# Kernel tuning notes

Measured on AMD Instinct MI355X. Metric: run time of the kernel, lower is better.

## Reference

```python
import jax, jax.numpy as jnp
import numpy as np

TEMPERATURE = 0.07
NEG_INF_FILL = -1e9  # matches torch fill_diagonal_(-1000000000.0)


def setup_inputs() -> dict:
    key = jax.random.key(0)
    feats = jax.random.normal(key, (6144, 768), dtype=jnp.float32)
    return {"feats": feats}


def reference(feats):
    # L2-normalize rows (torch F.normalize uses eps=1e-12 clamp on the norm)
    norm = jnp.maximum(jnp.linalg.norm(feats, axis=1, keepdims=True), 1e-12)
    f = feats / norm
    N = f.shape[0]
    sim = jnp.matmul(f, f.T) / TEMPERATURE            # [N, N]
    eye = jnp.eye(N, dtype=bool)
    sim = jnp.where(eye, NEG_INF_FILL, sim)           # fill diagonal
    labels = jnp.arange(N) // 3                       # 3 views per slice
    pos = (labels[:, None] == labels[None, :]) & ~eye  # positives, self excluded
    # masked logsumexp over positives via weights b (grad-safe masking)
    numerator = jax.scipy.special.logsumexp(sim, axis=1, b=pos.astype(sim.dtype))
    denominator = jax.scipy.special.logsumexp(sim, axis=1)
    loss = jnp.sum(-(numerator - denominator)) / N
    return loss
```

## Files before the change

kernel.cpp:

```cpp
#include <hip/hip_runtime.h>

#define NN 6144
#define DD 768
#define NB 48
#define NTILES 1176
#define INV_T 14.285714285714286f
#define CMAX  14.285714285714286f

typedef int i32x4 __attribute__((ext_vector_type(4)));
typedef int i32x8 __attribute__((ext_vector_type(8)));
typedef float f32x4_t __attribute__((ext_vector_type(4)));

__device__ __forceinline__ void load_lds16(const void* g, void* l) {
    __builtin_amdgcn_global_load_lds((__attribute__((address_space(1))) void*)g,
                                     (__attribute__((address_space(3))) void*)l,
                                     16, 0, 0);
}

__global__ void norm_kernel(const float* __restrict__ feats,
                            unsigned int* __restrict__ fb8,
                            float* __restrict__ den_num) {
    const int wid = threadIdx.x >> 6;
    const int lane = threadIdx.x & 63;
    const int row = blockIdx.x * 4 + wid;

    if (threadIdx.x < 8) den_num[blockIdx.x * 8 + threadIdx.x] = 0.0f;

    const float4* src = (const float4*)(feats + (size_t)row * DD);
    float4 v[3];
    float ss = 0.0f;
#pragma unroll
    for (int i = 0; i < 3; ++i) {
        v[i] = src[lane + i * 64];
        ss += v[i].x * v[i].x + v[i].y * v[i].y + v[i].z * v[i].z + v[i].w * v[i].w;
    }
#pragma unroll
    for (int m = 32; m >= 1; m >>= 1) ss += __shfl_xor(ss, m);
    const float sc = 1.0f / fmaxf(sqrtf(ss), 1e-12f);

#pragma unroll
    for (int i = 0; i < 3; ++i) {
        unsigned int w = 0;
        w = __builtin_amdgcn_cvt_pk_fp8_f32(v[i].x * sc, v[i].y * sc, w, 0);
        w = __builtin_amdgcn_cvt_pk_fp8_f32(v[i].z * sc, v[i].w * sc, w, 1);
        fb8[(size_t)row * 192 + lane + i * 64] = w;
    }
}

__global__ __launch_bounds__(256, 2) void gemm_expsum_kernel(
        const unsigned char* __restrict__ fb8,
        float* __restrict__ den_sum, float* __restrict__ num_sum) {
    __shared__ __align__(16) char sA0[128 * 128];
    __shared__ __align__(16) char sA1[128 * 128];
    __shared__ __align__(16) char sB0[128 * 128];
    __shared__ __align__(16) char sB1[128 * 128];

    int rem = blockIdx.x;
    int bi = 0, rowlen = NB;
    while (rem >= rowlen) { rem -= rowlen; rowlen--; bi++; }
    const int bj = bi + rem;
    const bool isdiag = (bi == bj);
    const bool neardiag = (bj - bi) <= 1;
    const int i0 = bi * 128;
    const int j0 = bj * 128;

    const int t = threadIdx.x;
    const int lane = t & 63;
    const int wid = t >> 6;
    const int wm = wid >> 1;
    const int wn = wid & 1;

    const int srow = t >> 3;
    const int scb = ((t & 7) ^ (srow & 7)) * 16;
    const unsigned char* gA = fb8 + (size_t)(i0 + srow) * DD + scb;
    const unsigned char* gB = fb8 + (size_t)(j0 + srow) * DD + scb;
    const int ldsoff = wid * 1024;

    f32x4_t acc[4][4];
    const f32x4_t zz = {0.0f, 0.0f, 0.0f, 0.0f};
#pragma unroll
    for (int mi = 0; mi < 4; ++mi)
#pragma unroll
        for (int ni = 0; ni < 4; ++ni) acc[mi][ni] = zz;

    const int q = lane >> 4;
    const int mrow = lane & 15;
    const int x7 = lane & 7;
    const int c0 = ((q << 1) ^ x7) << 4;
    const int c1 = (((q << 1) | 1) ^ x7) << 4;

#define STAGE(dstA, dstB, k0)                                                 \
    {                                                                         \
        _Pragma("unroll")                                                     \
        for (int i = 0; i < 4; ++i) {                                         \
            load_lds16(gA + (size_t)(i * 32) * DD + (k0), (dstA) + ldsoff + i * 4096); \
            load_lds16(gB + (size_t)(i * 32) * DD + (k0), (dstB) + ldsoff + i * 4096); \
        }                                                                     \
    }

#define COMPUTE(srcA, srcB)                                                   \
    {                                                                         \
        i32x8 af[4];                                                          \
        _Pragma("unroll")                                                     \
        for (int mi = 0; mi < 4; ++mi) {                                      \
            const char* p = (srcA) + (wm * 64 + mi * 16 + mrow) * 128;        \
            i32x4 lo = *(const i32x4*)(p + c0);                               \
            i32x4 hi = *(const i32x4*)(p + c1);                               \
            af[mi] = __builtin_shufflevector(lo, hi, 0, 1, 2, 3, 4, 5, 6, 7); \
        }                                                                     \
        _Pragma("unroll")                                                     \
        for (int ni = 0; ni < 4; ++ni) {                                      \
            const char* p = (srcB) + (wn * 64 + ni * 16 + mrow) * 128;        \
            i32x4 lo = *(const i32x4*)(p + c0);                               \
            i32x4 hi = *(const i32x4*)(p + c1);                               \
            i32x8 bf = __builtin_shufflevector(lo, hi, 0, 1, 2, 3, 4, 5, 6, 7); \
            _Pragma("unroll")                                                 \
            for (int mi = 0; mi < 4; ++mi)                                    \
                acc[mi][ni] = __builtin_amdgcn_mfma_scale_f32_16x16x128_f8f6f4( \
                    af[mi], bf, acc[mi][ni], 0, 0,                            \
                    0, 0x7F7F7F7F, 0, 0x7F7F7F7F);                            \
        }                                                                     \
    }

    STAGE(sA0, sB0, 0);
    __syncthreads();

#pragma unroll 1
    for (int kb = 0; kb < 2; ++kb) {
        const int k0 = kb * 256;
        STAGE(sA1, sB1, k0 + 128);
        COMPUTE(sA0, sB0);
        __syncthreads();
        STAGE(sA0, sB0, k0 + 256);
        COMPUTE(sA1, sB1);
        __syncthreads();
    }
    STAGE(sA1, sB1, 640);
    COMPUTE(sA0, sB0);
    __syncthreads();
    COMPUTE(sA1, sB1);

#undef STAGE
#undef COMPUTE

    const int colb = j0 + wn * 64 + mrow;
    const int rowb = i0 + wm * 64 + (q << 2);
    float cs[4] = {0.f, 0.f, 0.f, 0.f};
    float csn[4] = {0.f, 0.f, 0.f, 0.f};
#pragma unroll
    for (int mi = 0; mi < 4; ++mi) {
        float rsv[4] = {0.f, 0.f, 0.f, 0.f};
        float rsn[4] = {0.f, 0.f, 0.f, 0.f};
#pragma unroll
        for (int ni = 0; ni < 4; ++ni) {
            const int col = colb + ni * 16;
#pragma unroll
            for (int r = 0; r < 4; ++r) {
                const int row = rowb + mi * 16 + r;
                float e = __expf(__builtin_fmaf(acc[mi][ni][r], INV_T, -CMAX));
                if (isdiag && row == col) e = 0.0f;
                rsv[r] += e;
                cs[ni] += e;
                if (neardiag && (row / 3 == col / 3) && row != col) {
                    rsn[r] += e;
                    csn[ni] += e;
                }
            }
        }
#pragma unroll
        for (int r = 0; r < 4; ++r) {
            float v = rsv[r];
            v += __shfl_xor(v, 8);
            v += __shfl_xor(v, 4);
            v += __shfl_xor(v, 2);
            v += __shfl_xor(v, 1);
            if (mrow == 0) atomicAdd(&den_sum[rowb + mi * 16 + r], v);
        }
        if (neardiag) {
#pragma unroll
            for (int r = 0; r < 4; ++r) {
                float v = rsn[r];
                v += __shfl_xor(v, 8);
                v += __shfl_xor(v, 4);
                v += __shfl_xor(v, 2);
                v += __shfl_xor(v, 1);
                if (mrow == 0) atomicAdd(&num_sum[rowb + mi * 16 + r], v);
            }
        }
    }
    if (!isdiag) {
#pragma unroll
        for (int ni = 0; ni < 4; ++ni) {
            float v = cs[ni];
            v += __shfl_xor(v, 16);
            v += __shfl_xor(v, 32);
            if (q == 0) atomicAdd(&den_sum[colb + ni * 16], v);
        }
        if (neardiag) {
#pragma unroll
            for (int ni = 0; ni < 4; ++ni) {
                float v = csn[ni];
                v += __shfl_xor(v, 16);
                v += __shfl_xor(v, 32);
                if (q == 0) atomicAdd(&num_sum[colb + ni * 16], v);
            }
        }
    }
}

__global__ void finalize_kernel(const float* __restrict__ den_sum,
                                const float* __restrict__ num_sum,
                                float* __restrict__ out) {
    float local = 0.0f;
    for (int i = threadIdx.x; i < NN; i += 256) {
        local += logf(den_sum[i]) - logf(num_sum[i]);
    }
#pragma unroll
    for (int m = 32; m >= 1; m >>= 1) local += __shfl_xor(local, m);
    __shared__ float ws[4];
    if ((threadIdx.x & 63) == 0) ws[threadIdx.x >> 6] = local;
    __syncthreads();
    if (threadIdx.x == 0) out[0] = (ws[0] + ws[1] + ws[2] + ws[3]) / (float)NN;
}

extern "C" void kernel_launch(void* const* d_in, const int* in_sizes, int n_in,
                              void* d_out, int out_size, void* d_ws, size_t ws_size,
                              hipStream_t stream) {
    const float* feats = (const float*)d_in[0];
    float* out = (float*)d_out;

    char* ws = (char*)d_ws;
    unsigned int* fb8 = (unsigned int*)ws;
    float* den_num    = (float*)(ws + 4718592);
    float* den_sum    = den_num;
    float* num_sum    = den_num + NN;

    norm_kernel<<<NN / 4, 256, 0, stream>>>(feats, fb8, den_num);
    gemm_expsum_kernel<<<NTILES, 256, 0, stream>>>((const unsigned char*)fb8,
                                                   den_sum, num_sum);
    finalize_kernel<<<1, 256, 0, stream>>>(den_sum, num_sum, out);
}
```

Before: 115.6 us.

## Swizzle tile order into super-blocks and overlap loads via partial vmcnt waits

```diff
diff --git a/kernel.cpp b/kernel.cpp
--- a/kernel.cpp
+++ b/kernel.cpp
@@ -55,10 +55,28 @@
     __shared__ __align__(16) char sB0[128 * 128];
     __shared__ __align__(16) char sB1[128 * 128];
 
-    int rem = blockIdx.x;
-    int bi = 0, rowlen = NB;
-    while (rem >= rowlen) { rem -= rowlen; rowlen--; bi++; }
-    const int bj = bi + rem;
+    {
+    }
+    const int chunk = blockIdx.x & 7;
+    const int pos   = blockIdx.x >> 3;
+    int rem = chunk * 147 + pos;
+
+    int si = 0;
+    while (rem >= 510 - 144 * si) { rem -= 510 - 144 * si; ++si; }
+    int bi, bj;
+    if (rem < 78) {
+        int r = 0;
+        while (rem >= 12 - r) { rem -= 12 - r; ++r; }
+        bi = si * 12 + r;
+        bj = si * 12 + r + rem;
+    } else {
+        rem -= 78;
+        const int sj = si + 1 + rem / 144;
+        const int lo = rem % 144;
+        bi = si * 12 + lo / 12;
+        bj = sj * 12 + lo % 12;
+    }
+
     const bool isdiag = (bi == bj);
     const bool neardiag = (bj - bi) <= 1;
     const int i0 = bi * 128;
@@ -100,6 +118,7 @@
 
 #define COMPUTE(srcA, srcB)                                                   \
     {                                                                         \
+        __builtin_amdgcn_s_setprio(1);                                        \
         i32x8 af[4];                                                          \
         _Pragma("unroll")                                                     \
         for (int mi = 0; mi < 4; ++mi) {                                      \
@@ -120,28 +139,46 @@
                     af[mi], bf, acc[mi][ni], 0, 0,                            \
                     0, 0x7F7F7F7F, 0, 0x7F7F7F7F);                            \
         }                                                                     \
-    }
+        __builtin_amdgcn_s_setprio(0);                                        \
+    }
+
+#define WAITBAR_KEEP8                                                         \
+    asm volatile("s_waitcnt vmcnt(8)" ::: "memory");                          \
+    __builtin_amdgcn_s_barrier();
+
+#define WAITBAR_DRAIN                                                         \
+    asm volatile("s_waitcnt vmcnt(0)" ::: "memory");                          \
+    __builtin_amdgcn_s_barrier();
+
+#define ENDBAR                                                                \
+    asm volatile("" ::: "memory");                                            \
+    __builtin_amdgcn_s_barrier();
 
     STAGE(sA0, sB0, 0);
-    __syncthreads();
 
 #pragma unroll 1
     for (int kb = 0; kb < 2; ++kb) {
         const int k0 = kb * 256;
         STAGE(sA1, sB1, k0 + 128);
+        WAITBAR_KEEP8
         COMPUTE(sA0, sB0);
-        __syncthreads();
+        ENDBAR
         STAGE(sA0, sB0, k0 + 256);
+        WAITBAR_KEEP8
         COMPUTE(sA1, sB1);
-        __syncthreads();
+        ENDBAR
     }
     STAGE(sA1, sB1, 640);
+    WAITBAR_KEEP8
     COMPUTE(sA0, sB0);
-    __syncthreads();
+    WAITBAR_DRAIN
     COMPUTE(sA1, sB1);
 
 #undef STAGE
 #undef COMPUTE
+#undef WAITBAR_KEEP8
+#undef WAITBAR_DRAIN
+#undef ENDBAR
 
     const int colb = j0 + wn * 64 + mrow;
     const int rowb = i0 + wm * 64 + (q << 2);
```

After: 114.9 us. Within noise of the previous version (-0.6%).
